# Optimization experiments

Hardware: AMD Instinct MI355X
Metric: run time of the kernel (lower is better)

The kernel has to match this reference:

```python
import jax, jax.numpy as jnp
import numpy as np

# MoE config (matches init_kwargs): dim=512, num_experts=16, top_k=2, ffn mult=4
DIM = 512
NUM_EXPERTS = 16
TOP_K = 2
HIDDEN = 4 * DIM  # FeedForward inner dim
TOKENS = 2048
LN_EPS = 1e-5


def setup_inputs() -> dict:
    key = jax.random.key(0)
    ks = jax.random.split(key, 4)
    scaled = lambda k, shape, fan_in: (
        jax.random.normal(k, shape, dtype=jnp.float32) / np.sqrt(fan_in)
    )
    return {
        "x": jax.random.normal(ks[0], (TOKENS, DIM), dtype=jnp.float32),
        # gate: Linear(dim, num_experts, bias=False)
        "Wg": scaled(ks[1], (DIM, NUM_EXPERTS), DIM),
        # per-expert FFN params stacked on leading expert axis
        "W1": scaled(ks[2], (NUM_EXPERTS, DIM, HIDDEN), DIM),
        "b1": jnp.zeros((NUM_EXPERTS, HIDDEN), jnp.float32),
        "ln_g": jnp.ones((NUM_EXPERTS, HIDDEN), jnp.float32),
        "ln_b": jnp.zeros((NUM_EXPERTS, HIDDEN), jnp.float32),
        "W2": scaled(ks[3], (NUM_EXPERTS, HIDDEN, DIM), HIDDEN),
        "b2": jnp.zeros((NUM_EXPERTS, DIM), jnp.float32),
    }


def reference(x, Wg, W1, b1, ln_g, ln_b, W2, b2):
    # ---- routing ----
    gate_logits = x @ Wg                                   # [T, E]
    w, sel = jax.lax.top_k(gate_logits, TOP_K)             # [T, k]
    # softmax over the selected-experts axis, computed in fp32 (matches dtype=torch.float)
    w = jax.nn.softmax(w.astype(jnp.float32), axis=-1).astype(x.dtype)
    n_exp = Wg.shape[1]
    # combine[t, e] = sum_k w[t, k] * 1[sel[t, k] == e]
    combine = jnp.sum(
        w[..., None] * jax.nn.one_hot(sel, n_exp, dtype=x.dtype), axis=1
    )                                                      # [T, E]

    # ---- all experts (dense, jit-friendly dispatch) ----
    # FeedForward: Linear -> SiLU -> LayerNorm -> (Dropout=identity at eval) -> Linear
    h = jnp.einsum("td,edh->eth", x, W1) + b1[:, None, :]  # [E, T, H]
    h = jax.nn.silu(h)
    mu = jnp.mean(h, axis=-1, keepdims=True)
    var = jnp.mean(jnp.square(h - mu), axis=-1, keepdims=True)
    h = (h - mu) * jax.lax.rsqrt(var + LN_EPS)
    h = h * ln_g[:, None, :] + ln_b[:, None, :]
    y = jnp.einsum("eth,ehd->etd", h, W2) + b2[:, None, :]  # [E, T, D]

    # ---- weighted combine (scatter-add equivalent) ----
    return jnp.einsum("etd,te->td", y, combine)             # [T, D]
```

## Files before the change

kernel.cpp:

```cpp
#include <hip/hip_runtime.h>
#include <hip/hip_bf16.h>

#define TOKENS 2048
#define DIM 512
#define NEXP 16
#define HID 2048
#define CAP 320
#define NTPE (CAP / 64)
#define MTILES (NEXP * NTPE)
#define NROWS (NEXP * CAP)

typedef unsigned short ushort_t;
typedef __attribute__((ext_vector_type(8))) __bf16 bf16x8;
typedef __attribute__((ext_vector_type(4))) float f32x4;

#define OFF_CNT 0
#define OFF_LTOK 1024
#define OFF_LW 21504
#define OFF_S1 41984
#define OFF_S2 62464
#define OFF_XBF 82944
#define OFF_H 2180096
#define OFF_W1T 23151616
#define OFF_W2T 56706048

__device__ __forceinline__ ushort_t f2b(float f) {
  __bf16 b = (__bf16)f;
  return __builtin_bit_cast(unsigned short, b);
}
__device__ __forceinline__ float b2f(ushort_t u) {
  return __builtin_bit_cast(float, (unsigned)u << 16);
}

__global__ __launch_bounds__(256) void wconv_k(
    const float* __restrict__ W1, const float* __restrict__ W2,
    ushort_t* __restrict__ W1t, ushort_t* __restrict__ W2t,
    int* __restrict__ counts) {
  if (blockIdx.x == 0 && blockIdx.y == 0 && threadIdx.x < NEXP)
    counts[threadIdx.x] = 0;
  int bx = blockIdx.x;
  const float* src;
  ushort_t* dst;
  int K, N, nnt;
  if (bx < 1024) { src = W1; dst = W1t; K = DIM; N = HID; nnt = 64; }
  else { src = W2; dst = W2t; K = HID; N = DIM; nnt = 16; bx -= 1024; }
  int e = blockIdx.y;
  int kt = bx / nnt, ntb = bx % nnt;
  int k0 = kt * 32, n0 = ntb * 32;
  __shared__ ushort_t Ls[32 * 33];
  int t = threadIdx.x;
  int r = t >> 3, c4 = (t & 7) * 4;
  const float* sp = src + ((size_t)e * K + k0 + r) * N + n0 + c4;
  float4 v = *(const float4*)sp;
  Ls[r * 33 + c4 + 0] = f2b(v.x);
  Ls[r * 33 + c4 + 1] = f2b(v.y);
  Ls[r * 33 + c4 + 2] = f2b(v.z);
  Ls[r * 33 + c4 + 3] = f2b(v.w);
  __syncthreads();
  union { ushort_t u[4]; unsigned long long q; } o;
#pragma unroll
  for (int i = 0; i < 4; i++) o.u[i] = Ls[(c4 + i) * 33 + r];
  *(unsigned long long*)(dst + ((size_t)e * N + n0 + r) * K + k0 + c4) = o.q;
}

__global__ __launch_bounds__(256) void router_k(
    const float* __restrict__ x, const float* __restrict__ Wg,
    ushort_t* __restrict__ xbf, int* __restrict__ counts,
    int* __restrict__ ltok, float* __restrict__ lw,
    float* __restrict__ s1, float* __restrict__ s2, float* __restrict__ out) {
  int t = threadIdx.x;
  {
    float4 z = {0.f, 0.f, 0.f, 0.f};
    float4* o4 = (float4*)out + blockIdx.x * 4096 + t;
#pragma unroll
    for (int i = 0; i < 16; i++) o4[i * 256] = z;
  }
  {
    int idx = blockIdx.x * 256 + t;
    if (idx < NROWS) { s1[idx] = 0.f; s2[idx] = 0.f; }
  }

  __shared__ float xs[4][512];
  __shared__ float lg[4][16];
  __shared__ int lcnt[NEXP];
  __shared__ int ltoks[NEXP][64];
  __shared__ float lws[NEXP][64];
  __shared__ int base_s[NEXP];

  if (t < NEXP) lcnt[t] = 0;
  __syncthreads();

  int lane = t & 63, w = t >> 6;
  int dq = lane >> 2, e4 = lane & 3;
  const float* wgp = Wg + dq * NEXP + e4 * 4;

  for (int it = 0; it < 8; it++) {
    int tok = blockIdx.x * 32 + w * 8 + it;
    const float* xr = x + (size_t)tok * DIM + lane * 8;
    float4 xa = *(const float4*)xr;
    float4 xb = *(const float4*)(xr + 4);
    union { ushort_t u[8]; uint4 v; } pk;
    pk.u[0] = f2b(xa.x); pk.u[1] = f2b(xa.y); pk.u[2] = f2b(xa.z); pk.u[3] = f2b(xa.w);
    pk.u[4] = f2b(xb.x); pk.u[5] = f2b(xb.y); pk.u[6] = f2b(xb.z); pk.u[7] = f2b(xb.w);
    *(uint4*)(xbf + (size_t)tok * DIM + lane * 8) = pk.v;
    *(float4*)&xs[w][lane * 8] = xa;
    *(float4*)&xs[w][lane * 8 + 4] = xb;

    float4 a = {0.f, 0.f, 0.f, 0.f};
#pragma unroll
    for (int kk = 0; kk < 32; kk++) {
      float xv = xs[w][kk * 16 + dq];
      float4 g = *(const float4*)(wgp + kk * 16 * NEXP);
      a.x += xv * g.x; a.y += xv * g.y; a.z += xv * g.z; a.w += xv * g.w;
    }
#pragma unroll
    for (int off = 32; off >= 4; off >>= 1) {
      a.x += __shfl_down(a.x, off);
      a.y += __shfl_down(a.y, off);
      a.z += __shfl_down(a.z, off);
      a.w += __shfl_down(a.w, off);
    }
    if (lane < 4) *(float4*)&lg[w][lane * 4] = a;
    if (lane == 0) {
      int i0 = 0;
      float v0 = lg[w][0];
#pragma unroll
      for (int e = 1; e < NEXP; e++)
        if (lg[w][e] > v0) { v0 = lg[w][e]; i0 = e; }
      int i1 = -1;
      float v1 = -3.4e38f;
#pragma unroll
      for (int e = 0; e < NEXP; e++)
        if (e != i0 && lg[w][e] > v1) { v1 = lg[w][e]; i1 = e; }
      float ex = __expf(v1 - v0);
      float w0 = 1.f / (1.f + ex);
      int p0 = atomicAdd(&lcnt[i0], 1);
      ltoks[i0][p0] = tok;
      lws[i0][p0] = w0;
      int p1 = atomicAdd(&lcnt[i1], 1);
      ltoks[i1][p1] = tok;
      lws[i1][p1] = ex / (1.f + ex);
    }
  }
  __syncthreads();
  if (t < NEXP) base_s[t] = atomicAdd(&counts[t], lcnt[t]);
  __syncthreads();
  int e = t >> 4, i0 = t & 15;
  int n = lcnt[e], b = base_s[e];
  for (int i = i0; i < n; i += 16) {
    int slot = b + i;
    if (slot < CAP) {
      ltok[e * CAP + slot] = ltoks[e][i];
      lw[e * CAP + slot] = lws[e][i];
    }
  }
}

__global__ __launch_bounds__(256) void ffn1_k(
    const ushort_t* __restrict__ W1t, const float* __restrict__ b1,
    const int* __restrict__ counts, const int* __restrict__ ltok,
    const ushort_t* __restrict__ xbf, ushort_t* __restrict__ hbuf,
    float* __restrict__ s1, float* __restrict__ s2) {
  int e = blockIdx.x / NTPE, mt = blockIdx.x % NTPE;
  int cnt = counts[e];
  if (cnt - mt * 64 <= 0) return;
  int row0 = e * CAP + mt * 64;
  int h0 = blockIdx.y * 128;

  __shared__ __align__(16) ushort_t As[64 * 40];

  int t = threadIdx.x;
  int lane = t & 63, wave = t >> 6;
  int quad = lane >> 4, l16 = lane & 15;

  int sr = t >> 2, sp = t & 3;
  int stok = ltok[row0 + sr];
  const ushort_t* sx = xbf + (size_t)(stok < 0 ? 0 : stok) * DIM + sp * 8;
  bool sok = stok >= 0;

  int ncol = h0 + wave * 32 + l16;
  const ushort_t* bb = W1t + ((size_t)e * HID + ncol) * DIM + quad * 8;

  f32x4 acc[4][2];
#pragma unroll
  for (int a = 0; a < 4; a++)
#pragma unroll
    for (int b = 0; b < 2; b++) acc[a][b] = {0.f, 0.f, 0.f, 0.f};

  for (int ks = 0; ks < DIM / 32; ks++) {
    int kc = ks * 32;
    uint4 av = {0u, 0u, 0u, 0u};
    if (sok) av = *(const uint4*)(sx + kc);
    __syncthreads();
    *(uint4*)(&As[sr * 40 + sp * 8]) = av;

    bf16x8 bfr[2];
    bfr[0] = *(const bf16x8*)(bb + kc);
    bfr[1] = *(const bf16x8*)(bb + (size_t)16 * DIM + kc);
    __syncthreads();
    bf16x8 af[4];
#pragma unroll
    for (int mb = 0; mb < 4; mb++)
      af[mb] = *(const bf16x8*)(&As[(mb * 16 + l16) * 40 + quad * 8]);
#pragma unroll
    for (int mb = 0; mb < 4; mb++)
#pragma unroll
      for (int nb = 0; nb < 2; nb++)
        acc[mb][nb] = __builtin_amdgcn_mfma_f32_16x16x32_bf16(af[mb], bfr[nb], acc[mb][nb], 0, 0, 0);
  }

  float bia0 = b1[e * HID + ncol];
  float bia1 = b1[e * HID + ncol + 16];
#pragma unroll
  for (int mb = 0; mb < 4; mb++) {
#pragma unroll
    for (int i = 0; i < 4; i++) {
      int m = mb * 16 + quad * 4 + i;
      size_t rowg = (size_t)(row0 + m);
      float v0 = acc[mb][0][i] + bia0;
      v0 = v0 / (1.f + __expf(-v0));
      float v1 = acc[mb][1][i] + bia1;
      v1 = v1 / (1.f + __expf(-v1));
      hbuf[rowg * HID + ncol] = f2b(v0);
      hbuf[rowg * HID + ncol + 16] = f2b(v1);
      float ps = v0 + v1, qs = v0 * v0 + v1 * v1;
      ps += __shfl_down(ps, 8); qs += __shfl_down(qs, 8);
      ps += __shfl_down(ps, 4); qs += __shfl_down(qs, 4);
      ps += __shfl_down(ps, 2); qs += __shfl_down(qs, 2);
      ps += __shfl_down(ps, 1); qs += __shfl_down(qs, 1);
      if (l16 == 0) {
        atomicAdd(&s1[rowg], ps);
        atomicAdd(&s2[rowg], qs);
      }
    }
  }
}

__global__ __launch_bounds__(256) void ffn2_k(
    const ushort_t* __restrict__ W2t, const float* __restrict__ b2,
    const float* __restrict__ lng, const float* __restrict__ lnb,
    const int* __restrict__ counts, const int* __restrict__ ltok,
    const float* __restrict__ lw, const ushort_t* __restrict__ hbuf,
    const float* __restrict__ s1, const float* __restrict__ s2,
    float* __restrict__ out) {
  int e = blockIdx.x / NTPE, mt = blockIdx.x % NTPE;
  int cnt = counts[e];
  int valid = cnt - mt * 64;
  if (valid <= 0) return;
  valid = valid > 64 ? 64 : valid;
  int row0 = e * CAP + mt * 64;
  int n0 = blockIdx.y * 128;
  int kbeg = blockIdx.z * (HID / 2);

  __shared__ __align__(16) ushort_t As[64 * 40];

  int t = threadIdx.x;
  int lane = t & 63, wave = t >> 6;
  int quad = lane >> 4, l16 = lane & 15;

  int sr = t >> 2, sp = t & 3;
  size_t srow = (size_t)(row0 + sr);
  const ushort_t* hr = hbuf + srow * HID + kbeg + sp * 8;
  float smu = s1[srow] * (1.f / HID);
  float var = s2[srow] * (1.f / HID) - smu * smu;
  float srs = rsqrtf(var + 1e-5f);
  const float* gp = lng + (size_t)e * HID + kbeg + sp * 8;
  const float* cp = lnb + (size_t)e * HID + kbeg + sp * 8;

  int ncol = n0 + wave * 32 + l16;
  const ushort_t* bb = W2t + ((size_t)e * DIM + ncol) * HID + kbeg + quad * 8;

  f32x4 acc[4][2];
#pragma unroll
  for (int a = 0; a < 4; a++)
#pragma unroll
    for (int b = 0; b < 2; b++) acc[a][b] = {0.f, 0.f, 0.f, 0.f};

  for (int ks = 0; ks < (HID / 2) / 32; ks++) {
    int kc = ks * 32;
    union { uint4 v; ushort_t u[8]; } hv;
    hv.v = *(const uint4*)(hr + kc);
    float4 g0 = *(const float4*)(gp + kc);
    float4 g1 = *(const float4*)(gp + kc + 4);
    float4 c0 = *(const float4*)(cp + kc);
    float4 c1 = *(const float4*)(cp + kc + 4);
    union { ushort_t u[8]; uint4 v; } pk;
    {
      float gs[8] = {g0.x, g0.y, g0.z, g0.w, g1.x, g1.y, g1.z, g1.w};
      float cs[8] = {c0.x, c0.y, c0.z, c0.w, c1.x, c1.y, c1.z, c1.w};
#pragma unroll
      for (int j = 0; j < 8; j++) {
        float f = (b2f(hv.u[j]) - smu) * srs;
        pk.u[j] = f2b(f * gs[j] + cs[j]);
      }
    }
    __syncthreads();
    *(uint4*)(&As[sr * 40 + sp * 8]) = pk.v;

    bf16x8 bfr[2];
    bfr[0] = *(const bf16x8*)(bb + kc);
    bfr[1] = *(const bf16x8*)(bb + (size_t)16 * HID + kc);
    __syncthreads();
    bf16x8 af[4];
#pragma unroll
    for (int mb = 0; mb < 4; mb++)
      af[mb] = *(const bf16x8*)(&As[(mb * 16 + l16) * 40 + quad * 8]);
#pragma unroll
    for (int mb = 0; mb < 4; mb++)
#pragma unroll
      for (int nb = 0; nb < 2; nb++)
        acc[mb][nb] = __builtin_amdgcn_mfma_f32_16x16x32_bf16(af[mb], bfr[nb], acc[mb][nb], 0, 0, 0);
  }

  bool addb = (blockIdx.z == 0);
#pragma unroll
  for (int mb = 0; mb < 4; mb++) {
#pragma unroll
    for (int i = 0; i < 4; i++) {
      int m = mb * 16 + quad * 4 + i;
      if (m < valid) {
        int tok = ltok[row0 + m];
        float w = lw[row0 + m];
#pragma unroll
        for (int nb = 0; nb < 2; nb++) {
          int n = ncol + nb * 16;
          float v = acc[mb][nb][i] + (addb ? b2[e * DIM + n] : 0.f);
          atomicAdd(out + (size_t)tok * DIM + n, w * v);
        }
      }
    }
  }
}

extern "C" void kernel_launch(void* const* d_in, const int* in_sizes, int n_in,
                              void* d_out, int out_size, void* d_ws, size_t ws_size,
                              hipStream_t stream) {
  const float* x = (const float*)d_in[0];
  const float* Wg = (const float*)d_in[1];
  const float* W1 = (const float*)d_in[2];
  const float* b1 = (const float*)d_in[3];
  const float* lng = (const float*)d_in[4];
  const float* lnb = (const float*)d_in[5];
  const float* W2 = (const float*)d_in[6];
  const float* b2 = (const float*)d_in[7];
  float* out = (float*)d_out;

  char* ws = (char*)d_ws;
  int* counts = (int*)(ws + OFF_CNT);
  int* ltok = (int*)(ws + OFF_LTOK);
  float* lw = (float*)(ws + OFF_LW);
  float* s1 = (float*)(ws + OFF_S1);
  float* s2 = (float*)(ws + OFF_S2);
  ushort_t* xbf = (ushort_t*)(ws + OFF_XBF);
  ushort_t* hbuf = (ushort_t*)(ws + OFF_H);
  ushort_t* W1t = (ushort_t*)(ws + OFF_W1T);
  ushort_t* W2t = (ushort_t*)(ws + OFF_W2T);

  wconv_k<<<dim3(2048, NEXP), 256, 0, stream>>>(W1, W2, W1t, W2t, counts);
  router_k<<<64, 256, 0, stream>>>(x, Wg, xbf, counts, ltok, lw, s1, s2, out);
  ffn1_k<<<dim3(MTILES, HID / 128), 256, 0, stream>>>(W1t, b1, counts, ltok, xbf, hbuf, s1, s2);
  ffn2_k<<<dim3(MTILES, DIM / 128, 2), 256, 0, stream>>>(W2t, b2, lng, lnb, counts, ltok,
                                                         lw, hbuf, s1, s2, out);
}
```

Measured before the change: 279.5 us.

## Double-buffer GEMM tiles, widen N tiles, and batch weight-transpose work per block

```diff
diff --git a/kernel.cpp b/kernel.cpp
--- a/kernel.cpp
+++ b/kernel.cpp
@@ -41,26 +41,34 @@
   int bx = blockIdx.x;
   const float* src;
   ushort_t* dst;
-  int K, N, nnt;
-  if (bx < 1024) { src = W1; dst = W1t; K = DIM; N = HID; nnt = 64; }
-  else { src = W2; dst = W2t; K = HID; N = DIM; nnt = 16; bx -= 1024; }
+  int K, N, nnc;
+  if (bx < 256) { src = W1; dst = W1t; K = DIM; N = HID; nnc = 16; }
+  else { src = W2; dst = W2t; K = HID; N = DIM; nnc = 4; bx -= 256; }
   int e = blockIdx.y;
-  int kt = bx / nnt, ntb = bx % nnt;
-  int k0 = kt * 32, n0 = ntb * 32;
-  __shared__ ushort_t Ls[32 * 33];
+  int kt = bx / nnc, nb = bx % nnc;
+  int k0 = kt * 32, n0 = nb * 128;
+  __shared__ ushort_t Ls[2][32 * 33];
   int t = threadIdx.x;
   int r = t >> 3, c4 = (t & 7) * 4;
   const float* sp = src + ((size_t)e * K + k0 + r) * N + n0 + c4;
+  ushort_t* dp = dst + ((size_t)e * N + n0 + r) * K + k0 + c4;
   float4 v = *(const float4*)sp;
-  Ls[r * 33 + c4 + 0] = f2b(v.x);
-  Ls[r * 33 + c4 + 1] = f2b(v.y);
-  Ls[r * 33 + c4 + 2] = f2b(v.z);
-  Ls[r * 33 + c4 + 3] = f2b(v.w);
-  __syncthreads();
-  union { ushort_t u[4]; unsigned long long q; } o;
-#pragma unroll
-  for (int i = 0; i < 4; i++) o.u[i] = Ls[(c4 + i) * 33 + r];
-  *(unsigned long long*)(dst + ((size_t)e * N + n0 + r) * K + k0 + c4) = o.q;
+#pragma unroll
+  for (int j = 0; j < 4; j++) {
+    ushort_t* L = Ls[j & 1];
+    L[r * 33 + c4 + 0] = f2b(v.x);
+    L[r * 33 + c4 + 1] = f2b(v.y);
+    L[r * 33 + c4 + 2] = f2b(v.z);
+    L[r * 33 + c4 + 3] = f2b(v.w);
+    float4 vn;
+    if (j < 3) vn = *(const float4*)(sp + (j + 1) * 32);
+    __syncthreads();
+    union { ushort_t u[4]; unsigned long long q; } o;
+#pragma unroll
+    for (int i = 0; i < 4; i++) o.u[i] = L[(c4 + i) * 33 + r];
+    *(unsigned long long*)(dp + (size_t)(j * 32) * K) = o.q;
+    v = vn;
+  }
 }
 
 __global__ __launch_bounds__(256) void router_k(
@@ -165,9 +173,9 @@
   int cnt = counts[e];
   if (cnt - mt * 64 <= 0) return;
   int row0 = e * CAP + mt * 64;
-  int h0 = blockIdx.y * 128;
-
-  __shared__ __align__(16) ushort_t As[64 * 40];
+  int h0 = blockIdx.y * 256;
+
+  __shared__ __align__(16) ushort_t As[2][64 * 40];
 
   int t = threadIdx.x;
   int lane = t & 63, wave = t >> 6;
@@ -175,55 +183,80 @@
 
   int sr = t >> 2, sp = t & 3;
   int stok = ltok[row0 + sr];
-  const ushort_t* sx = xbf + (size_t)(stok < 0 ? 0 : stok) * DIM + sp * 8;
-  bool sok = stok >= 0;
-
-  int ncol = h0 + wave * 32 + l16;
+  bool sok = (unsigned)stok < TOKENS;
+  const ushort_t* sx = xbf + (size_t)(sok ? stok : 0) * DIM + sp * 8;
+
+  int ncol = h0 + wave * 64 + l16;
   const ushort_t* bb = W1t + ((size_t)e * HID + ncol) * DIM + quad * 8;
 
-  f32x4 acc[4][2];
+  f32x4 acc[4][4];
 #pragma unroll
   for (int a = 0; a < 4; a++)
 #pragma unroll
-    for (int b = 0; b < 2; b++) acc[a][b] = {0.f, 0.f, 0.f, 0.f};
-
-  for (int ks = 0; ks < DIM / 32; ks++) {
-    int kc = ks * 32;
-    uint4 av = {0u, 0u, 0u, 0u};
-    if (sok) av = *(const uint4*)(sx + kc);
+    for (int b = 0; b < 4; b++) acc[a][b] = {0.f, 0.f, 0.f, 0.f};
+
+  uint4 avB = {0u, 0u, 0u, 0u};
+  {
+    uint4 avA = {0u, 0u, 0u, 0u};
+    if (sok) {
+      avA = *(const uint4*)(sx);
+      avB = *(const uint4*)(sx + 32);
+    }
+    *(uint4*)(&As[0][sr * 40 + sp * 8]) = avA;
+  }
+  bf16x8 bc[4];
+#pragma unroll
+  for (int nb = 0; nb < 4; nb++)
+    bc[nb] = *(const bf16x8*)(bb + (size_t)nb * 16 * DIM);
+
+#pragma unroll
+  for (int ks = 0; ks < 16; ks++) {
     __syncthreads();
-    *(uint4*)(&As[sr * 40 + sp * 8]) = av;
-
-    bf16x8 bfr[2];
-    bfr[0] = *(const bf16x8*)(bb + kc);
-    bfr[1] = *(const bf16x8*)(bb + (size_t)16 * DIM + kc);
-    __syncthreads();
+    bf16x8 bn[4];
+    if (ks < 15) {
+#pragma unroll
+      for (int nb = 0; nb < 4; nb++)
+        bn[nb] = *(const bf16x8*)(bb + (size_t)nb * 16 * DIM + (ks + 1) * 32);
+    }
+    uint4 avN = {0u, 0u, 0u, 0u};
+    if (ks < 14 && sok) avN = *(const uint4*)(sx + (ks + 2) * 32);
+
     bf16x8 af[4];
 #pragma unroll
     for (int mb = 0; mb < 4; mb++)
-      af[mb] = *(const bf16x8*)(&As[(mb * 16 + l16) * 40 + quad * 8]);
+      af[mb] = *(const bf16x8*)(&As[ks & 1][(mb * 16 + l16) * 40 + quad * 8]);
 #pragma unroll
     for (int mb = 0; mb < 4; mb++)
 #pragma unroll
-      for (int nb = 0; nb < 2; nb++)
-        acc[mb][nb] = __builtin_amdgcn_mfma_f32_16x16x32_bf16(af[mb], bfr[nb], acc[mb][nb], 0, 0, 0);
-  }
-
-  float bia0 = b1[e * HID + ncol];
-  float bia1 = b1[e * HID + ncol + 16];
+      for (int nb = 0; nb < 4; nb++)
+        acc[mb][nb] = __builtin_amdgcn_mfma_f32_16x16x32_bf16(af[mb], bc[nb], acc[mb][nb], 0, 0, 0);
+
+    if (ks < 15) {
+      *(uint4*)(&As[(ks + 1) & 1][sr * 40 + sp * 8]) = avB;
+      avB = avN;
+#pragma unroll
+      for (int nb = 0; nb < 4; nb++) bc[nb] = bn[nb];
+    }
+  }
+
+  float bia[4];
+#pragma unroll
+  for (int nb = 0; nb < 4; nb++) bia[nb] = b1[e * HID + ncol + nb * 16];
 #pragma unroll
   for (int mb = 0; mb < 4; mb++) {
 #pragma unroll
     for (int i = 0; i < 4; i++) {
       int m = mb * 16 + quad * 4 + i;
       size_t rowg = (size_t)(row0 + m);
-      float v0 = acc[mb][0][i] + bia0;
-      v0 = v0 / (1.f + __expf(-v0));
-      float v1 = acc[mb][1][i] + bia1;
-      v1 = v1 / (1.f + __expf(-v1));
-      hbuf[rowg * HID + ncol] = f2b(v0);
-      hbuf[rowg * HID + ncol + 16] = f2b(v1);
-      float ps = v0 + v1, qs = v0 * v0 + v1 * v1;
+      float ps = 0.f, qs = 0.f;
+#pragma unroll
+      for (int nb = 0; nb < 4; nb++) {
+        float v = acc[mb][nb][i] + bia[nb];
+        v = v / (1.f + __expf(-v));
+        hbuf[rowg * HID + ncol + nb * 16] = f2b(v);
+        ps += v;
+        qs += v * v;
+      }
       ps += __shfl_down(ps, 8); qs += __shfl_down(qs, 8);
       ps += __shfl_down(ps, 4); qs += __shfl_down(qs, 4);
       ps += __shfl_down(ps, 2); qs += __shfl_down(qs, 2);
@@ -249,14 +282,19 @@
   if (valid <= 0) return;
   valid = valid > 64 ? 64 : valid;
   int row0 = e * CAP + mt * 64;
-  int n0 = blockIdx.y * 128;
+  int n0 = blockIdx.y * 256;
   int kbeg = blockIdx.z * (HID / 2);
 
-  __shared__ __align__(16) ushort_t As[64 * 40];
+  __shared__ __align__(16) ushort_t As[2][64 * 40];
+  __shared__ float Gs[1024];
+  __shared__ float Cs[1024];
 
   int t = threadIdx.x;
   int lane = t & 63, wave = t >> 6;
   int quad = lane >> 4, l16 = lane & 15;
+
+  *(float4*)&Gs[t * 4] = *(const float4*)(lng + (size_t)e * HID + kbeg + t * 4);
+  *(float4*)&Cs[t * 4] = *(const float4*)(lnb + (size_t)e * HID + kbeg + t * 4);
 
   int sr = t >> 2, sp = t & 3;
   size_t srow = (size_t)(row0 + sr);
@@ -264,55 +302,81 @@
   float smu = s1[srow] * (1.f / HID);
   float var = s2[srow] * (1.f / HID) - smu * smu;
   float srs = rsqrtf(var + 1e-5f);
-  const float* gp = lng + (size_t)e * HID + kbeg + sp * 8;
-  const float* cp = lnb + (size_t)e * HID + kbeg + sp * 8;
-
-  int ncol = n0 + wave * 32 + l16;
+
+  int ncol = n0 + wave * 64 + l16;
   const ushort_t* bb = W2t + ((size_t)e * DIM + ncol) * HID + kbeg + quad * 8;
 
-  f32x4 acc[4][2];
+  f32x4 acc[4][4];
 #pragma unroll
   for (int a = 0; a < 4; a++)
 #pragma unroll
-    for (int b = 0; b < 2; b++) acc[a][b] = {0.f, 0.f, 0.f, 0.f};
-
-  for (int ks = 0; ks < (HID / 2) / 32; ks++) {
-    int kc = ks * 32;
+    for (int b = 0; b < 4; b++) acc[a][b] = {0.f, 0.f, 0.f, 0.f};
+
+  uint4 hvA = *(const uint4*)(hr);
+  uint4 hvB = *(const uint4*)(hr + 32);
+  __syncthreads();
+
+  {
     union { uint4 v; ushort_t u[8]; } hv;
-    hv.v = *(const uint4*)(hr + kc);
-    float4 g0 = *(const float4*)(gp + kc);
-    float4 g1 = *(const float4*)(gp + kc + 4);
-    float4 c0 = *(const float4*)(cp + kc);
-    float4 c1 = *(const float4*)(cp + kc + 4);
+    hv.v = hvA;
+    int sb = sp * 8;
     union { ushort_t u[8]; uint4 v; } pk;
-    {
-      float gs[8] = {g0.x, g0.y, g0.z, g0.w, g1.x, g1.y, g1.z, g1.w};
-      float cs[8] = {c0.x, c0.y, c0.z, c0.w, c1.x, c1.y, c1.z, c1.w};
+#pragma unroll
+    for (int j = 0; j < 8; j++) {
+      float f = (b2f(hv.u[j]) - smu) * srs;
+      pk.u[j] = f2b(f * Gs[sb + j] + Cs[sb + j]);
+    }
+    *(uint4*)(&As[0][sr * 40 + sp * 8]) = pk.v;
+  }
+  bf16x8 bc[4];
+#pragma unroll
+  for (int nb = 0; nb < 4; nb++)
+    bc[nb] = *(const bf16x8*)(bb + (size_t)nb * 16 * HID);
+
+#pragma unroll 8
+  for (int ks = 0; ks < 32; ks++) {
+    __syncthreads();
+    bf16x8 bn[4];
+    if (ks < 31) {
+#pragma unroll
+      for (int nb = 0; nb < 4; nb++)
+        bn[nb] = *(const bf16x8*)(bb + (size_t)nb * 16 * HID + (ks + 1) * 32);
+    }
+    uint4 hvN = {0u, 0u, 0u, 0u};
+    if (ks < 30) hvN = *(const uint4*)(hr + (ks + 2) * 32);
+
+    bf16x8 af[4];
+#pragma unroll
+    for (int mb = 0; mb < 4; mb++)
+      af[mb] = *(const bf16x8*)(&As[ks & 1][(mb * 16 + l16) * 40 + quad * 8]);
+#pragma unroll
+    for (int mb = 0; mb < 4; mb++)
+#pragma unroll
+      for (int nb = 0; nb < 4; nb++)
+        acc[mb][nb] = __builtin_amdgcn_mfma_f32_16x16x32_bf16(af[mb], bc[nb], acc[mb][nb], 0, 0, 0);
+
+    if (ks < 31) {
+      union { uint4 v; ushort_t u[8]; } hv;
+      hv.v = hvB;
+      int sb = (ks + 1) * 32 + sp * 8;
+      union { ushort_t u[8]; uint4 v; } pk;
 #pragma unroll
       for (int j = 0; j < 8; j++) {
         float f = (b2f(hv.u[j]) - smu) * srs;
-        pk.u[j] = f2b(f * gs[j] + cs[j]);
+        pk.u[j] = f2b(f * Gs[sb + j] + Cs[sb + j]);
       }
-    }
-    __syncthreads();
-    *(uint4*)(&As[sr * 40 + sp * 8]) = pk.v;
-
-    bf16x8 bfr[2];
-    bfr[0] = *(const bf16x8*)(bb + kc);
-    bfr[1] = *(const bf16x8*)(bb + (size_t)16 * HID + kc);
-    __syncthreads();
-    bf16x8 af[4];
-#pragma unroll
-    for (int mb = 0; mb < 4; mb++)
-      af[mb] = *(const bf16x8*)(&As[(mb * 16 + l16) * 40 + quad * 8]);
-#pragma unroll
-    for (int mb = 0; mb < 4; mb++)
-#pragma unroll
-      for (int nb = 0; nb < 2; nb++)
-        acc[mb][nb] = __builtin_amdgcn_mfma_f32_16x16x32_bf16(af[mb], bfr[nb], acc[mb][nb], 0, 0, 0);
+      *(uint4*)(&As[(ks + 1) & 1][sr * 40 + sp * 8]) = pk.v;
+      hvB = hvN;
+#pragma unroll
+      for (int nb = 0; nb < 4; nb++) bc[nb] = bn[nb];
+    }
   }
 
   bool addb = (blockIdx.z == 0);
+  float bia[4];
+#pragma unroll
+  for (int nb = 0; nb < 4; nb++)
+    bia[nb] = addb ? b2[e * DIM + ncol + nb * 16] : 0.f;
 #pragma unroll
   for (int mb = 0; mb < 4; mb++) {
 #pragma unroll
@@ -322,10 +386,9 @@
         int tok = ltok[row0 + m];
         float w = lw[row0 + m];
 #pragma unroll
-        for (int nb = 0; nb < 2; nb++) {
-          int n = ncol + nb * 16;
-          float v = acc[mb][nb][i] + (addb ? b2[e * DIM + n] : 0.f);
-          atomicAdd(out + (size_t)tok * DIM + n, w * v);
+        for (int nb = 0; nb < 4; nb++) {
+          float v = acc[mb][nb][i] + bia[nb];
+          atomicAdd(out + (size_t)tok * DIM + ncol + nb * 16, w * v);
         }
       }
     }
@@ -356,9 +419,9 @@
   ushort_t* W1t = (ushort_t*)(ws + OFF_W1T);
   ushort_t* W2t = (ushort_t*)(ws + OFF_W2T);
 
-  wconv_k<<<dim3(2048, NEXP), 256, 0, stream>>>(W1, W2, W1t, W2t, counts);
+  wconv_k<<<dim3(512, NEXP), 256, 0, stream>>>(W1, W2, W1t, W2t, counts);
   router_k<<<64, 256, 0, stream>>>(x, Wg, xbf, counts, ltok, lw, s1, s2, out);
-  ffn1_k<<<dim3(MTILES, HID / 128), 256, 0, stream>>>(W1t, b1, counts, ltok, xbf, hbuf, s1, s2);
-  ffn2_k<<<dim3(MTILES, DIM / 128, 2), 256, 0, stream>>>(W2t, b2, lng, lnb, counts, ltok,
+  ffn1_k<<<dim3(MTILES, HID / 256), 256, 0, stream>>>(W1t, b1, counts, ltok, xbf, hbuf, s1, s2);
+  ffn2_k<<<dim3(MTILES, DIM / 256, 2), 256, 0, stream>>>(W2t, b2, lng, lnb, counts, ltok,
                                                          lw, hbuf, s1, s2, out);
 }
```

Result: slower. 288.8 us (+3.3%).
